# Performance work log

Hardware: AMD Instinct MI355X
Metric: run time of the kernel (lower is better)

## Reference

```python
import jax, jax.numpy as jnp
import numpy as np

B, S, D = 4, 2048, 1024

def setup_inputs() -> dict:
    key = jax.random.key(0)
    kx, kq, kk, kv = jax.random.split(key, 4)
    glorot = (6.0 / (D + D)) ** 0.5
    return {
        "x": jax.random.normal(kx, (B, S, D), dtype=jnp.float32),
        "Wq": jax.random.uniform(kq, (D, D), jnp.float32, -glorot, glorot),
        "Wk": jax.random.uniform(kk, (D, D), jnp.float32, -glorot, glorot),
        "Wv": jax.random.uniform(kv, (D, D), jnp.float32, -glorot, glorot),
    }

def reference(x, Wq, Wk, Wv):
    # q,k,v: [B,S,D]
    q = jnp.einsum("bsd,de->bse", x, Wq)
    k = jnp.einsum("bsd,de->bse", x, Wk)
    v = jnp.einsum("bsd,de->bse", x, Wv)
    scale = jnp.sqrt(jnp.asarray(q.shape[-1], q.dtype))
    scores = jnp.einsum("bqd,bkd->bqk", q, k) / scale  # [B,S,S]
    w = jax.nn.softmax(scores, axis=-1)
    return jnp.einsum("bqk,bkd->bqd", w, v)
```

## Files before the change

kernel.cpp:

```cpp
#include <hip/hip_runtime.h>
#include <hip/hip_bf16.h>


typedef _Float16 half_t;
typedef _Float16 half8 __attribute__((ext_vector_type(8)));
typedef _Float16 half4v __attribute__((ext_vector_type(4)));
typedef float f32x4 __attribute__((ext_vector_type(4)));

__device__ __forceinline__ void load16_to_lds(const half_t* g, half_t* l) {
  __builtin_amdgcn_global_load_lds(
      (const __attribute__((address_space(1))) void*)g,
      (__attribute__((address_space(3))) void*)l, 16, 0, 0);
}

#define LGKM0 asm volatile("s_waitcnt lgkmcnt(0)" ::: "memory")
#define LGKM8 asm volatile("s_waitcnt lgkmcnt(8)" ::: "memory")
#define VM0   asm volatile("s_waitcnt vmcnt(0)" ::: "memory")
#define VM4   asm volatile("s_waitcnt vmcnt(4)" ::: "memory")
#define VM6   asm volatile("s_waitcnt vmcnt(6)" ::: "memory")
#define BAR   __builtin_amdgcn_s_barrier()
#define PRIO1 __builtin_amdgcn_s_setprio(1)
#define PRIO0 __builtin_amdgcn_s_setprio(0)

__global__ __launch_bounds__(512, 2) void qkvt_gemm8(
    const half_t* __restrict__ xh, const half_t* __restrict__ wt,
    half_t* __restrict__ qk, half_t* __restrict__ vtg) {
  __shared__ __align__(16) half_t As[2][256 * 64];
  __shared__ __align__(16) half_t Bs[2][256 * 64];

  const int b = blockIdx.x;
  const int x = b & 7, j = b >> 3;
  const int m0 = (x * 4 + (j & 3)) * 256;
  const int n0 = (j >> 2) * 256;

  const int t     = threadIdx.x;
  const int lane  = t & 63;
  const int wave  = t >> 6;
  const int wr128 = (wave >> 2) * 128;
  const int wc64  = (wave & 3) * 64;
  const int lm    = lane & 15;
  const int lq    = lane >> 4;
  const int pos0  = (lq ^ (lm & 7)) * 8;
  const int pos1  = ((4 + lq) ^ (lm & 7)) * 8;
  const int t8    = t * 8;

  const int trow = t >> 3;
  const int tchk = (t & 7) ^ (trow & 7);
  const half_t* gA0 = xh + (size_t)(m0 + trow) * 1024 + tchk * 8;
  const half_t* gB0 = wt + (size_t)(n0 + trow) * 1024 + tchk * 8;

  f32x4 acc[8][4] = {};
  half8 va[4][2], vb0[2][2], vb1[2][2];

#define ST_A(buf, h, kt) do {                                                  \
    load16_to_lds(gA0 + (size_t)((h)*128) * 1024 + (size_t)(kt) * 64,          \
                  &As[buf][(h)*128*64] + t8);                                  \
    load16_to_lds(gA0 + (size_t)((h)*128+64) * 1024 + (size_t)(kt) * 64,       \
                  &As[buf][((h)*128+64)*64] + t8);                             \
  } while (0)
#define ST_B(buf, h, kt) do {                                                  \
    load16_to_lds(gB0 + (size_t)((h)*128) * 1024 + (size_t)(kt) * 64,          \
                  &Bs[buf][(h)*128*64] + t8);                                  \
    load16_to_lds(gB0 + (size_t)((h)*128+64) * 1024 + (size_t)(kt) * 64,       \
                  &Bs[buf][((h)*128+64)*64] + t8);                             \
  } while (0)
#define RD_A(buf, mh) do {                                                     \
    _Pragma("unroll") for (int m = 0; m < 4; ++m) {                            \
      const int ar = wr128 + (mh)*64 + m * 16 + lm;                            \
      va[m][0] = *(const half8*)&As[buf][ar * 64 + pos0];                      \
      va[m][1] = *(const half8*)&As[buf][ar * 64 + pos1];                      \
    } } while (0)
#define RD_B(buf, nh, vb) do {                                                 \
    _Pragma("unroll") for (int n = 0; n < 2; ++n) {                            \
      const int br = wc64 + (nh)*32 + n * 16 + lm;                             \
      vb[n][0] = *(const half8*)&Bs[buf][br * 64 + pos0];                      \
      vb[n][1] = *(const half8*)&Bs[buf][br * 64 + pos1];                      \
    } } while (0)
#define MF_Q(mh, nh, vb) do {                                                  \
    _Pragma("unroll") for (int kk = 0; kk < 2; ++kk)                           \
    _Pragma("unroll") for (int m = 0; m < 4; ++m)                              \
    _Pragma("unroll") for (int n = 0; n < 2; ++n)                              \
      acc[(mh)*4+m][(nh)*2+n] = __builtin_amdgcn_mfma_f32_16x16x32_f16(        \
          va[m][kk], vb[n][kk], acc[(mh)*4+m][(nh)*2+n], 0, 0, 0);             \
  } while (0)

  ST_A(0, 0, 0); ST_A(0, 1, 0);
  ST_B(0, 0, 0); ST_B(0, 1, 0);
  ST_B(1, 0, 1); ST_B(1, 1, 1);
  VM4;
  BAR;

#pragma unroll 1
  for (int i = 0; i < 8; ++i) {
    const int st1 = (2 * i + 1 < 15) ? 2 * i + 1 : 15;
    const int st2 = (2 * i + 2 < 15) ? 2 * i + 2 : 15;
    const int st3 = (2 * i + 3 < 15) ? 2 * i + 3 : 15;
    RD_A(0, 0); RD_B(0, 0, vb0);
    ST_A(1, 0, st1);
    LGKM8;
    BAR; LGKM0;
    PRIO1; MF_Q(0, 0, vb0); PRIO0;
    BAR;
    RD_B(0, 1, vb1);
    ST_A(1, 1, st1);
    BAR; LGKM0;
    PRIO1; MF_Q(0, 1, vb1); PRIO0;
    BAR;
    RD_A(0, 1);
    ST_B(0, 0, st2);
    BAR; LGKM0;
    PRIO1; MF_Q(1, 0, vb0); PRIO0;
    BAR;
    ST_B(0, 1, st2);
    BAR; LGKM0;
    PRIO1; MF_Q(1, 1, vb1); PRIO0;
    VM4;
    BAR;
    RD_A(1, 0); RD_B(1, 0, vb0);
    ST_A(0, 0, st2);
    LGKM8;
    BAR; LGKM0;
    PRIO1; MF_Q(0, 0, vb0); PRIO0;
    BAR;
    RD_B(1, 1, vb1);
    ST_A(0, 1, st2);
    BAR; LGKM0;
    PRIO1; MF_Q(0, 1, vb1); PRIO0;
    BAR;
    RD_A(1, 1);
    ST_B(1, 0, st3);
    BAR; LGKM0;
    PRIO1; MF_Q(1, 0, vb0); PRIO0;
    BAR;
    ST_B(1, 1, st3);
    BAR; LGKM0;
    PRIO1; MF_Q(1, 1, vb1); PRIO0;
    VM4;
    BAR;
  }

#pragma unroll
  for (int m = 0; m < 8; ++m)
#pragma unroll
    for (int n = 0; n < 4; ++n) {
      const int col = n0 + wc64 + n * 16 + lm;
#pragma unroll
      for (int r = 0; r < 4; ++r) {
        const int row = m0 + wr128 + m * 16 + lq * 4 + r;
        qk[(size_t)row * 2048 + col] = (half_t)acc[m][n][r];
      }
    }
#undef ST_A
#undef ST_B
#undef RD_A
#undef RD_B
#undef MF_Q

  const int m0v = (j >> 2) * 128;
  const int n0v = (x * 4 + (j & 3)) * 256;
  const int wmv = (wave >> 2) * 64;
  const int wnv = (wave & 3) * 64;

  const half_t* gA2 = wt + (size_t)2 * 1024 * 1024 +
                      (size_t)(m0v + trow) * 1024 + tchk * 8;
  const half_t* gB2 = xh + (size_t)(n0v + trow) * 1024 + tchk * 8;

  f32x4 acc2[4][4] = {};

#define ST_A2(buf, kt) do {                                                    \
    load16_to_lds(gA2 + (size_t)(kt) * 64, &As[buf][0] + t8);                  \
    load16_to_lds(gA2 + (size_t)64 * 1024 + (size_t)(kt) * 64,                 \
                  &As[buf][64*64] + t8);                                       \
  } while (0)
#define ST_B2(buf, h, kt) do {                                                 \
    load16_to_lds(gB2 + (size_t)((h)*128) * 1024 + (size_t)(kt) * 64,          \
                  &Bs[buf][(h)*128*64] + t8);                                  \
    load16_to_lds(gB2 + (size_t)((h)*128+64) * 1024 + (size_t)(kt) * 64,       \
                  &Bs[buf][((h)*128+64)*64] + t8);                             \
  } while (0)
#define RD_A2(buf, mh) do {                                                    \
    _Pragma("unroll") for (int m = 0; m < 2; ++m) {                            \
      const int ar = wmv + (mh)*32 + m * 16 + lm;                              \
      va[(mh)*2+m][0] = *(const half8*)&As[buf][ar * 64 + pos0];               \
      va[(mh)*2+m][1] = *(const half8*)&As[buf][ar * 64 + pos1];               \
    } } while (0)
#define RD_B2(buf, nh, vb) do {                                                \
    _Pragma("unroll") for (int n = 0; n < 2; ++n) {                            \
      const int br = wnv + (nh)*32 + n * 16 + lm;                              \
      vb[n][0] = *(const half8*)&Bs[buf][br * 64 + pos0];                      \
      vb[n][1] = *(const half8*)&Bs[buf][br * 64 + pos1];                      \
    } } while (0)
#define MF_V(mh, nh, vb) do {                                                  \
    _Pragma("unroll") for (int kk = 0; kk < 2; ++kk)                           \
    _Pragma("unroll") for (int m = 0; m < 2; ++m)                              \
    _Pragma("unroll") for (int n = 0; n < 2; ++n)                              \
      acc2[(mh)*2+m][(nh)*2+n] = __builtin_amdgcn_mfma_f32_16x16x32_f16(       \
          va[(mh)*2+m][kk], vb[n][kk], acc2[(mh)*2+m][(nh)*2+n], 0, 0, 0);     \
  } while (0)

  VM0;
  ST_B2(0, 0, 0); ST_B2(0, 1, 0); ST_A2(0, 0);
  ST_B2(1, 0, 1); ST_B2(1, 1, 1); ST_A2(1, 1);
  VM6;
  BAR;

#pragma unroll 1
  for (int i = 0; i < 8; ++i) {
    const int t2 = (2 * i + 2 < 15) ? 2 * i + 2 : 15;
    const int t3 = (2 * i + 3 < 15) ? 2 * i + 3 : 15;
    RD_A2(0, 0); RD_B2(0, 0, vb0);
    BAR; LGKM0;
    PRIO1; MF_V(0, 0, vb0); PRIO0;
    BAR;
    RD_B2(0, 1, vb1);
    BAR; LGKM0;
    PRIO1; MF_V(0, 1, vb1); PRIO0;
    BAR;
    RD_A2(0, 1);
    ST_B2(0, 0, t2);
    BAR; LGKM0;
    PRIO1; MF_V(1, 0, vb0); PRIO0;
    BAR;
    ST_B2(0, 1, t2); ST_A2(0, t2);
    BAR; LGKM0;
    PRIO1; MF_V(1, 1, vb1); PRIO0;
    VM6;
    BAR;
    RD_A2(1, 0); RD_B2(1, 0, vb0);
    BAR; LGKM0;
    PRIO1; MF_V(0, 0, vb0); PRIO0;
    BAR;
    RD_B2(1, 1, vb1);
    BAR; LGKM0;
    PRIO1; MF_V(0, 1, vb1); PRIO0;
    BAR;
    RD_A2(1, 1);
    ST_B2(1, 0, t3);
    BAR; LGKM0;
    PRIO1; MF_V(1, 0, vb0); PRIO0;
    BAR;
    ST_B2(1, 1, t3); ST_A2(1, t3);
    BAR; LGKM0;
    PRIO1; MF_V(1, 1, vb1); PRIO0;
    VM6;
    BAR;
  }

#pragma unroll
  for (int m = 0; m < 4; ++m)
#pragma unroll
    for (int n = 0; n < 4; ++n) {
      const int col = n0v + wnv + n * 16 + lm;
#pragma unroll
      for (int r = 0; r < 4; ++r) {
        const int row = m0v + wmv + m * 16 + lq * 4 + r;
        vtg[(size_t)row * 8192 + col] = (half_t)acc2[m][n][r];
      }
    }
#undef ST_A2
#undef ST_B2
#undef RD_A2
#undef RD_B2
#undef MF_V
}

__global__ __launch_bounds__(512, 2) void scores_gemm8(
    const half_t* __restrict__ qk, half_t* __restrict__ sc,
    float* __restrict__ lpart) {
  __shared__ __align__(16) half_t As[2][256 * 64];
  __shared__ __align__(16) half_t Bs[2][256 * 64];

  const int id  = blockIdx.x;
  const int x   = id & 7, j = id >> 3;
  const int bx  = j & 7;
  const int z   = x >> 1;
  const int by  = (x & 1) * 4 + (j >> 3);
  const int m0  = by * 256;
  const int n0  = bx * 256;
  const half_t* A  = qk + (size_t)z * 2048 * 2048;
  const half_t* Bm = A + 1024;
  half_t* C = sc + (size_t)z * 2048 * 2048;

  const int t     = threadIdx.x;
  const int lane  = t & 63;
  const int wave  = t >> 6;
  const int wr128 = (wave >> 2) * 128;
  const int wc64  = (wave & 3) * 64;
  const int lm    = lane & 15;
  const int lq    = lane >> 4;
  const int pos0  = (lq ^ (lm & 7)) * 8;
  const int pos1  = ((4 + lq) ^ (lm & 7)) * 8;
  const int t8    = t * 8;

  const int trow = t >> 3;
  const int tchk = (t & 7) ^ (trow & 7);
  const half_t* gA0 = A  + (size_t)(m0 + trow) * 2048 + tchk * 8;
  const half_t* gB0 = Bm + (size_t)(n0 + trow) * 2048 + tchk * 8;

  f32x4 acc[8][4] = {};
  half8 va[4][2], vb0[2][2], vb1[2][2];

#define ST_A(buf, h, kt) do {                                                  \
    load16_to_lds(gA0 + (size_t)((h)*128) * 2048 + (size_t)(kt) * 64,          \
                  &As[buf][(h)*128*64] + t8);                                  \
    load16_to_lds(gA0 + (size_t)((h)*128+64) * 2048 + (size_t)(kt) * 64,       \
                  &As[buf][((h)*128+64)*64] + t8);                             \
  } while (0)
#define ST_B(buf, h, kt) do {                                                  \
    load16_to_lds(gB0 + (size_t)((h)*128) * 2048 + (size_t)(kt) * 64,          \
                  &Bs[buf][(h)*128*64] + t8);                                  \
    load16_to_lds(gB0 + (size_t)((h)*128+64) * 2048 + (size_t)(kt) * 64,       \
                  &Bs[buf][((h)*128+64)*64] + t8);                             \
  } while (0)
#define RD_A(buf, mh) do {                                                     \
    _Pragma("unroll") for (int m = 0; m < 4; ++m) {                            \
      const int ar = wr128 + (mh)*64 + m * 16 + lm;                            \
      va[m][0] = *(const half8*)&As[buf][ar * 64 + pos0];                      \
      va[m][1] = *(const half8*)&As[buf][ar * 64 + pos1];                      \
    } } while (0)
#define RD_B(buf, nh, vb) do {                                                 \
    _Pragma("unroll") for (int n = 0; n < 2; ++n) {                            \
      const int br = wc64 + (nh)*32 + n * 16 + lm;                             \
      vb[n][0] = *(const half8*)&Bs[buf][br * 64 + pos0];                      \
      vb[n][1] = *(const half8*)&Bs[buf][br * 64 + pos1];                      \
    } } while (0)
#define MF_Q(mh, nh, vb) do {                                                  \
    _Pragma("unroll") for (int kk = 0; kk < 2; ++kk)                           \
    _Pragma("unroll") for (int m = 0; m < 4; ++m)                              \
    _Pragma("unroll") for (int n = 0; n < 2; ++n)                              \
      acc[(mh)*4+m][(nh)*2+n] = __builtin_amdgcn_mfma_f32_16x16x32_f16(        \
          va[m][kk], vb[n][kk], acc[(mh)*4+m][(nh)*2+n], 0, 0, 0);             \
  } while (0)

  ST_A(0, 0, 0); ST_A(0, 1, 0);
  ST_B(0, 0, 0); ST_B(0, 1, 0);
  ST_B(1, 0, 1); ST_B(1, 1, 1);
  VM4;
  BAR;

#pragma unroll 1
  for (int i = 0; i < 8; ++i) {
    const int st1 = (2 * i + 1 < 15) ? 2 * i + 1 : 15;
    const int st2 = (2 * i + 2 < 15) ? 2 * i + 2 : 15;
    const int st3 = (2 * i + 3 < 15) ? 2 * i + 3 : 15;
    RD_A(0, 0); RD_B(0, 0, vb0);
    ST_A(1, 0, st1);
    LGKM8;
    BAR; LGKM0;
    PRIO1; MF_Q(0, 0, vb0); PRIO0;
    BAR;
    RD_B(0, 1, vb1);
    ST_A(1, 1, st1);
    BAR; LGKM0;
    PRIO1; MF_Q(0, 1, vb1); PRIO0;
    BAR;
    RD_A(0, 1);
    ST_B(0, 0, st2);
    BAR; LGKM0;
    PRIO1; MF_Q(1, 0, vb0); PRIO0;
    BAR;
    ST_B(0, 1, st2);
    BAR; LGKM0;
    PRIO1; MF_Q(1, 1, vb1); PRIO0;
    VM4;
    BAR;
    RD_A(1, 0); RD_B(1, 0, vb0);
    ST_A(0, 0, st2);
    LGKM8;
    BAR; LGKM0;
    PRIO1; MF_Q(0, 0, vb0); PRIO0;
    BAR;
    RD_B(1, 1, vb1);
    ST_A(0, 1, st2);
    BAR; LGKM0;
    PRIO1; MF_Q(0, 1, vb1); PRIO0;
    BAR;
    RD_A(1, 1);
    ST_B(1, 0, st3);
    BAR; LGKM0;
    PRIO1; MF_Q(1, 0, vb0); PRIO0;
    BAR;
    ST_B(1, 1, st3);
    BAR; LGKM0;
    PRIO1; MF_Q(1, 1, vb1); PRIO0;
    VM4;
    BAR;
  }

  const float scale = 1.0f / 32.0f;
#pragma unroll
  for (int m = 0; m < 8; ++m)
#pragma unroll
    for (int r = 0; r < 4; ++r) {
      const int row = m0 + wr128 + m * 16 + lq * 4 + r;
      float s = 0.f;
#pragma unroll
      for (int n = 0; n < 4; ++n) {
        const int col = n0 + wc64 + n * 16 + lm;
        float v = __expf(acc[m][n][r] * scale - 8.0f);
        s += v;
        C[(size_t)row * 2048 + col] = (half_t)v;
      }
      s += __shfl_xor(s, 1); s += __shfl_xor(s, 2);
      s += __shfl_xor(s, 4); s += __shfl_xor(s, 8);
      if (lm == 0)
        lpart[((size_t)z * 2048 + row) * 32 + bx * 4 + (wave & 3)] = s;
    }
#undef ST_A
#undef ST_B
#undef RD_A
#undef RD_B
#undef MF_Q
}

__global__ __launch_bounds__(256) void pv_gemm(
    const half_t* __restrict__ sc, const half_t* __restrict__ vtg,
    float* __restrict__ out, const float* __restrict__ lpart) {
  __shared__ __align__(16) half_t As[128 * 64];
  __shared__ __align__(16) half_t Bs[128 * 64];
  __shared__ float linv[128];

  const int z  = blockIdx.z;
  const int m0 = blockIdx.x * 128;
  const int n0 = blockIdx.y * 128;
  const half_t* A  = sc  + (size_t)z * 2048 * 2048;
  const half_t* Bm = vtg + (size_t)z * 2048;
  float* C = out + (size_t)z * 2048 * 1024;
  constexpr int lda = 2048, ldb = 8192, ldc = 1024, K = 2048;

  const int t    = threadIdx.x;
  const int wave = t >> 6;
  const int lane = t & 63;
  const int wm   = (wave >> 1) * 64;
  const int wn   = (wave & 1) * 64;
  const int lm   = lane & 15;
  const int lq   = lane >> 4;
  const int lswz = lm & 7;

  if (t < 128) {
    const float4* lp = (const float4*)&lpart[((size_t)z * 2048 + m0 + t) * 32];
    float s = 0.f;
#pragma unroll
    for (int p = 0; p < 8; ++p) {
      float4 v = lp[p];
      s += v.x + v.y + v.z + v.w;
    }
    linv[t] = 1.0f / s;
  }

  const int trow = t >> 3;
  const int tchk = (t & 7) ^ (trow & 7);

  const half_t* gA0 = A  + (size_t)(m0 + trow) * lda + tchk * 8;
  const half_t* gB0 = Bm + (size_t)(n0 + trow) * ldb + tchk * 8;
  const size_t stepA = (size_t)32 * lda;
  const size_t stepB = (size_t)32 * ldb;

  half_t* lA0 = &As[t * 8];
  half_t* lB0 = &Bs[t * 8];

  f32x4 acc[4][4] = {};

  for (int k0 = 0; k0 < K; k0 += 64) {
    __syncthreads();
#pragma unroll
    for (int n = 0; n < 4; ++n) {
      load16_to_lds(gA0 + n * stepA + k0, lA0 + n * 2048);
      load16_to_lds(gB0 + n * stepB + k0, lB0 + n * 2048);
    }
    __syncthreads();

#pragma unroll
    for (int kk = 0; kk < 2; ++kk) {
      const int pos = ((kk * 4 + lq) ^ lswz) * 8;
      half8 a[4], bf[4];
#pragma unroll
      for (int i = 0; i < 4; ++i)
        a[i] = *(const half8*)&As[(wm + i * 16 + lm) * 64 + pos];
#pragma unroll
      for (int j = 0; j < 4; ++j)
        bf[j] = *(const half8*)&Bs[(wn + j * 16 + lm) * 64 + pos];
#pragma unroll
      for (int i = 0; i < 4; ++i)
#pragma unroll
        for (int j = 0; j < 4; ++j)
          acc[i][j] = __builtin_amdgcn_mfma_f32_16x16x32_f16(a[i], bf[j], acc[i][j], 0, 0, 0);
    }
  }

#pragma unroll
  for (int i = 0; i < 4; ++i)
#pragma unroll
    for (int r = 0; r < 4; ++r) {
      const int lrow = wm + i * 16 + lq * 4 + r;
      const float inv = linv[lrow];
      const int row = m0 + lrow;
#pragma unroll
      for (int j = 0; j < 4; ++j) {
        const int col = n0 + wn + j * 16 + lm;
        C[(size_t)row * ldc + col] = acc[i][j][r] * inv;
      }
    }
}

__global__ __launch_bounds__(256) void prep(
    const float* __restrict__ x, half_t* __restrict__ xh,
    const float* __restrict__ Wq, const float* __restrict__ Wk,
    const float* __restrict__ Wv, half_t* __restrict__ wt) {
  __shared__ half_t tile[32][33];
  const int b = blockIdx.x;
  const int t = threadIdx.x;
  if (b < 8192) {
    const int i = (b * 256 + t) * 4;
    const float4 v = *reinterpret_cast<const float4*>(x + i);
    half4v o;
    o.x = (half_t)v.x; o.y = (half_t)v.y; o.z = (half_t)v.z; o.w = (half_t)v.w;
    *reinterpret_cast<half4v*>(xh + i) = o;
  } else {
    int bb = b - 8192;
    const int w = bb >> 10; bb &= 1023;
    const float* in = (w == 0) ? Wq : (w == 1) ? Wk : Wv;
    half_t* o = wt + (size_t)w * 1024 * 1024;
    const int r0 = (bb >> 5) * 32, c0 = (bb & 31) * 32;
    const int tx = t & 31, ty = t >> 5;
#pragma unroll
    for (int i = 0; i < 32; i += 8)
      tile[ty + i][tx] = (half_t)in[(size_t)(r0 + ty + i) * 1024 + c0 + tx];
    __syncthreads();
#pragma unroll
    for (int i = 0; i < 32; i += 8)
      o[(size_t)(c0 + ty + i) * 1024 + r0 + tx] = tile[tx][ty + i];
  }
}

extern "C" void kernel_launch(void* const* d_in, const int* in_sizes, int n_in,
                              void* d_out, int out_size, void* d_ws, size_t ws_size,
                              hipStream_t stream) {
  constexpr int Bb = 4, S = 2048, D = 1024;
  constexpr size_t MS = (size_t)Bb * S;

  const float* x  = (const float*)d_in[0];
  const float* Wq = (const float*)d_in[1];
  const float* Wk = (const float*)d_in[2];
  const float* Wv = (const float*)d_in[3];
  float* out = (float*)d_out;

  char* p = (char*)d_ws;
  half_t* xh    = (half_t*)p; p += MS * D * 2;
  half_t* wt    = (half_t*)p; p += (size_t)3 * D * D * 2;
  half_t* qk    = (half_t*)p; p += MS * (size_t)(2 * D) * 2;
  half_t* vtg   = (half_t*)p; p += (size_t)D * MS * 2;
  half_t* sc    = (half_t*)p; p += (size_t)Bb * S * S * 2;
  float*  lpart = (float*)p;  p += MS * 32 * 4;

  prep<<<11264, 256, 0, stream>>>(x, xh, Wq, Wk, Wv, wt);
  qkvt_gemm8<<<256, 512, 0, stream>>>(xh, wt, qk, vtg);
  scores_gemm8<<<256, 512, 0, stream>>>(qk, sc, lpart);
  pv_gemm<<<dim3(16, 8, Bb), 256, 0, stream>>>(sc, vtg, out, lpart);
}
```

Before: 223.6 us.

## Rewrite PV GEMM as 8-wave double-buffered pipelined kernel with 128x256 tiles

Replaces the simple single-buffered 256-thread PV GEMM with an 8-wave, 128x256-tile kernel that double-buffers LDS and interleaves global-to-LDS loads with MFMA phases under barrier/priority scheduling, mirroring the other GEMM kernels. It also remaps block indices so blocks of the same batch share A/B tiles. The aim is to hide load latency behind MFMA and increase per-block reuse, at the cost of more LDS and a more fragile hand-tuned schedule.

```diff
diff --git a/kernel.cpp b/kernel.cpp
--- a/kernel.cpp
+++ b/kernel.cpp
@@ -413,29 +413,32 @@
 #undef MF_Q
 }
 
-__global__ __launch_bounds__(256) void pv_gemm(
+__global__ __launch_bounds__(512, 2) void pv_gemm8(
     const half_t* __restrict__ sc, const half_t* __restrict__ vtg,
     float* __restrict__ out, const float* __restrict__ lpart) {
-  __shared__ __align__(16) half_t As[128 * 64];
-  __shared__ __align__(16) half_t Bs[128 * 64];
+  __shared__ __align__(16) half_t As[2][128 * 64];
+  __shared__ __align__(16) half_t Bs[2][256 * 64];
   __shared__ float linv[128];
 
-  const int z  = blockIdx.z;
-  const int m0 = blockIdx.x * 128;
-  const int n0 = blockIdx.y * 128;
+  const int id = blockIdx.x;
+  const int x  = id & 7, j = id >> 3;
+  const int z  = x >> 1;
+  const int m0 = ((x & 1) * 8 + (j >> 2)) * 128;
+  const int n0 = (j & 3) * 256;
   const half_t* A  = sc  + (size_t)z * 2048 * 2048;
   const half_t* Bm = vtg + (size_t)z * 2048;
   float* C = out + (size_t)z * 2048 * 1024;
-  constexpr int lda = 2048, ldb = 8192, ldc = 1024, K = 2048;
 
   const int t    = threadIdx.x;
+  const int lane = t & 63;
   const int wave = t >> 6;
-  const int lane = t & 63;
-  const int wm   = (wave >> 1) * 64;
-  const int wn   = (wave & 1) * 64;
+  const int wmv  = (wave >> 2) * 64;
+  const int wnv  = (wave & 3) * 64;
   const int lm   = lane & 15;
   const int lq   = lane >> 4;
-  const int lswz = lm & 7;
+  const int pos0 = (lq ^ (lm & 7)) * 8;
+  const int pos1 = ((4 + lq) ^ (lm & 7)) * 8;
+  const int t8   = t * 8;
 
   if (t < 128) {
     const float4* lp = (const float4*)&lpart[((size_t)z * 2048 + m0 + t) * 32];
@@ -450,57 +453,108 @@
 
   const int trow = t >> 3;
   const int tchk = (t & 7) ^ (trow & 7);
-
-  const half_t* gA0 = A  + (size_t)(m0 + trow) * lda + tchk * 8;
-  const half_t* gB0 = Bm + (size_t)(n0 + trow) * ldb + tchk * 8;
-  const size_t stepA = (size_t)32 * lda;
-  const size_t stepB = (size_t)32 * ldb;
-
-  half_t* lA0 = &As[t * 8];
-  half_t* lB0 = &Bs[t * 8];
-
-  f32x4 acc[4][4] = {};
-
-  for (int k0 = 0; k0 < K; k0 += 64) {
-    __syncthreads();
-#pragma unroll
-    for (int n = 0; n < 4; ++n) {
-      load16_to_lds(gA0 + n * stepA + k0, lA0 + n * 2048);
-      load16_to_lds(gB0 + n * stepB + k0, lB0 + n * 2048);
-    }
-    __syncthreads();
-
-#pragma unroll
-    for (int kk = 0; kk < 2; ++kk) {
-      const int pos = ((kk * 4 + lq) ^ lswz) * 8;
-      half8 a[4], bf[4];
-#pragma unroll
-      for (int i = 0; i < 4; ++i)
-        a[i] = *(const half8*)&As[(wm + i * 16 + lm) * 64 + pos];
-#pragma unroll
-      for (int j = 0; j < 4; ++j)
-        bf[j] = *(const half8*)&Bs[(wn + j * 16 + lm) * 64 + pos];
-#pragma unroll
-      for (int i = 0; i < 4; ++i)
-#pragma unroll
-        for (int j = 0; j < 4; ++j)
-          acc[i][j] = __builtin_amdgcn_mfma_f32_16x16x32_f16(a[i], bf[j], acc[i][j], 0, 0, 0);
-    }
+  const half_t* gA2 = A  + (size_t)(m0 + trow) * 2048 + tchk * 8;
+  const half_t* gB2 = Bm + (size_t)(n0 + trow) * 8192 + tchk * 8;
+
+  f32x4 acc2[4][4] = {};
+  half8 va[4][2], vb0[2][2], vb1[2][2];
+
+#define ST_A2(buf, kt) do {                                                    \
+    load16_to_lds(gA2 + (size_t)(kt) * 64, &As[buf][0] + t8);                  \
+    load16_to_lds(gA2 + (size_t)64 * 2048 + (size_t)(kt) * 64,                 \
+                  &As[buf][64*64] + t8);                                       \
+  } while (0)
+#define ST_B2(buf, h, kt) do {                                                 \
+    load16_to_lds(gB2 + (size_t)((h)*128) * 8192 + (size_t)(kt) * 64,          \
+                  &Bs[buf][(h)*128*64] + t8);                                  \
+    load16_to_lds(gB2 + (size_t)((h)*128+64) * 8192 + (size_t)(kt) * 64,       \
+                  &Bs[buf][((h)*128+64)*64] + t8);                             \
+  } while (0)
+#define RD_A2(buf, mh) do {                                                    \
+    _Pragma("unroll") for (int m = 0; m < 2; ++m) {                            \
+      const int ar = wmv + (mh)*32 + m * 16 + lm;                              \
+      va[(mh)*2+m][0] = *(const half8*)&As[buf][ar * 64 + pos0];               \
+      va[(mh)*2+m][1] = *(const half8*)&As[buf][ar * 64 + pos1];               \
+    } } while (0)
+#define RD_B2(buf, nh, vb) do {                                                \
+    _Pragma("unroll") for (int n = 0; n < 2; ++n) {                            \
+      const int br = wnv + (nh)*32 + n * 16 + lm;                              \
+      vb[n][0] = *(const half8*)&Bs[buf][br * 64 + pos0];                      \
+      vb[n][1] = *(const half8*)&Bs[buf][br * 64 + pos1];                      \
+    } } while (0)
+#define MF_V(mh, nh, vb) do {                                                  \
+    _Pragma("unroll") for (int kk = 0; kk < 2; ++kk)                           \
+    _Pragma("unroll") for (int m = 0; m < 2; ++m)                              \
+    _Pragma("unroll") for (int n = 0; n < 2; ++n)                              \
+      acc2[(mh)*2+m][(nh)*2+n] = __builtin_amdgcn_mfma_f32_16x16x32_f16(       \
+          va[(mh)*2+m][kk], vb[n][kk], acc2[(mh)*2+m][(nh)*2+n], 0, 0, 0);     \
+  } while (0)
+
+  ST_B2(0, 0, 0); ST_B2(0, 1, 0); ST_A2(0, 0);
+  ST_B2(1, 0, 1); ST_B2(1, 1, 1); ST_A2(1, 1);
+  VM6;
+  BAR;
+
+#pragma unroll 1
+  for (int i = 0; i < 16; ++i) {
+    const int t2 = (2 * i + 2 < 31) ? 2 * i + 2 : 31;
+    const int t3 = (2 * i + 3 < 31) ? 2 * i + 3 : 31;
+    RD_A2(0, 0); RD_B2(0, 0, vb0);
+    BAR; LGKM0;
+    PRIO1; MF_V(0, 0, vb0); PRIO0;
+    BAR;
+    RD_B2(0, 1, vb1);
+    BAR; LGKM0;
+    PRIO1; MF_V(0, 1, vb1); PRIO0;
+    BAR;
+    RD_A2(0, 1);
+    ST_B2(0, 0, t2);
+    BAR; LGKM0;
+    PRIO1; MF_V(1, 0, vb0); PRIO0;
+    BAR;
+    ST_B2(0, 1, t2); ST_A2(0, t2);
+    BAR; LGKM0;
+    PRIO1; MF_V(1, 1, vb1); PRIO0;
+    VM6;
+    BAR;
+    RD_A2(1, 0); RD_B2(1, 0, vb0);
+    BAR; LGKM0;
+    PRIO1; MF_V(0, 0, vb0); PRIO0;
+    BAR;
+    RD_B2(1, 1, vb1);
+    BAR; LGKM0;
+    PRIO1; MF_V(0, 1, vb1); PRIO0;
+    BAR;
+    RD_A2(1, 1);
+    ST_B2(1, 0, t3);
+    BAR; LGKM0;
+    PRIO1; MF_V(1, 0, vb0); PRIO0;
+    BAR;
+    ST_B2(1, 1, t3); ST_A2(1, t3);
+    BAR; LGKM0;
+    PRIO1; MF_V(1, 1, vb1); PRIO0;
+    VM6;
+    BAR;
   }
 
 #pragma unroll
-  for (int i = 0; i < 4; ++i)
+  for (int m = 0; m < 4; ++m)
 #pragma unroll
     for (int r = 0; r < 4; ++r) {
-      const int lrow = wm + i * 16 + lq * 4 + r;
+      const int lrow = wmv + m * 16 + lq * 4 + r;
       const float inv = linv[lrow];
       const int row = m0 + lrow;
 #pragma unroll
-      for (int j = 0; j < 4; ++j) {
-        const int col = n0 + wn + j * 16 + lm;
-        C[(size_t)row * ldc + col] = acc[i][j][r] * inv;
+      for (int n = 0; n < 4; ++n) {
+        const int col = n0 + wnv + n * 16 + lm;
+        C[(size_t)row * 1024 + col] = acc2[m][n][r] * inv;
       }
     }
+#undef ST_A2
+#undef ST_B2
+#undef RD_A2
+#undef RD_B2
+#undef MF_V
 }
 
 __global__ __launch_bounds__(256) void prep(
@@ -556,5 +610,5 @@
   prep<<<11264, 256, 0, stream>>>(x, xh, Wq, Wk, Wv, wt);
   qkvt_gemm8<<<256, 512, 0, stream>>>(xh, wt, qk, vtg);
   scores_gemm8<<<256, 512, 0, stream>>>(qk, sc, lpart);
-  pv_gemm<<<dim3(16, 8, Bb), 256, 0, stream>>>(sc, vtg, out, lpart);
+  pv_gemm8<<<256, 512, 0, stream>>>(sc, vtg, out, lpart);
 }
```

New measurement: 220.7 us (median of 2 runs). Within noise of the previous version (-1.3%).
